# Kernel optimization log

Measured on AMD Instinct MI355X. Metric: run time of the kernel, lower is better.

## Reference

```python
import jax, jax.numpy as jnp
import numpy as np

N_HEADS = 16
N_KV_HEADS = 4
HEAD_DIM = 128  # d_model // n_heads = 2048 // 16
ROPE_THETA = 10000.0


def _rope_cos_sin(T, D, dtype):
    inv_freq = 1.0 / (ROPE_THETA ** (jnp.arange(0, D, 2, dtype=jnp.float32) / D))
    t = jnp.arange(T, dtype=jnp.float32)
    freqs = jnp.outer(t, inv_freq)               # [T, D/2]
    emb = jnp.concatenate([freqs, freqs], axis=-1)  # [T, D]
    return jnp.cos(emb).astype(dtype), jnp.sin(emb).astype(dtype)


def _rotate_half(x):
    x1, x2 = jnp.split(x, 2, axis=-1)
    return jnp.concatenate([-x2, x1], axis=-1)


def setup_inputs() -> dict:
    key = jax.random.key(0)
    k1, k2, k3, k4, k5 = jax.random.split(key, 5)
    B, T, C = 2, 2048, 2048
    H, KV, D = N_HEADS, N_KV_HEADS, HEAD_DIM
    s = 0.02
    return {
        "x": jax.random.normal(k1, (B, T, C), dtype=jnp.float32),
        "Wq": jax.random.normal(k2, (C, H * D), dtype=jnp.float32) * s,
        "Wk": jax.random.normal(k3, (C, KV * D), dtype=jnp.float32) * s,
        "Wv": jax.random.normal(k4, (C, KV * D), dtype=jnp.float32) * s,
        "Wo": jax.random.normal(k5, (H * D, C), dtype=jnp.float32) * s,
    }


def reference(x, Wq, Wk, Wv, Wo):
    B, T, C = x.shape
    H, KV, D = N_HEADS, N_KV_HEADS, HEAD_DIM
    G = H // KV
    scale = D ** -0.5

    q = (x @ Wq).reshape(B, T, H, D).transpose(0, 2, 1, 3)    # [B,H,T,D]
    k = (x @ Wk).reshape(B, T, KV, D).transpose(0, 2, 1, 3)   # [B,KV,T,D]
    v = (x @ Wv).reshape(B, T, KV, D).transpose(0, 2, 1, 3)   # [B,KV,T,D]

    cos, sin = _rope_cos_sin(T, D, x.dtype)  # [T,D] each, broadcasts over B,H
    q = q * cos + _rotate_half(q) * sin
    k = k * cos + _rotate_half(k) * sin

    # repeat_interleave kv heads to match query heads
    k = jnp.repeat(k, G, axis=1)  # [B,H,T,D]
    v = jnp.repeat(v, G, axis=1)  # [B,H,T,D]

    scores = jnp.einsum('bhqd,bhkd->bhqk', q, k) * scale  # [B,H,T,T]
    causal = jnp.tril(jnp.ones((T, T), dtype=bool))
    scores = jnp.where(causal, scores, jnp.finfo(scores.dtype).min)
    attn = jax.nn.softmax(scores, axis=-1)

    out = jnp.einsum('bhqk,bhkd->bhqd', attn, v)           # [B,H,T,D]
    out = out.transpose(0, 2, 1, 3).reshape(B, T, H * D)    # [B,T,C]
    return out @ Wo
```

## Files before the change

kernel.cpp:

```cpp
#include <hip/hip_runtime.h>
#include <cstdint>
#include <cstddef>

typedef __attribute__((ext_vector_type(4))) float f32x4;
typedef __attribute__((ext_vector_type(8))) short s16x8;
typedef __attribute__((ext_vector_type(4))) short s16x4;

#define B_  2
#define T_  2048
#define C_  2048
#define H_  16
#define KV_ 4
#define D_  128
#define M_  4096

static __device__ __forceinline__ float bf2f(ushort u){
  union { float f; uint32_t u; } x; x.u = ((uint32_t)u) << 16; return x.f;
}
static __device__ __forceinline__ ushort f2bf(float f){
  union { float f; uint32_t u; } x; x.f = f;
  uint32_t r = x.u + 0x7FFF + ((x.u >> 16) & 1);
  return (ushort)(r >> 16);
}

static __device__ __forceinline__ void gl_lds16(const ushort* g, ushort* s){
  __builtin_amdgcn_global_load_lds((const __attribute__((address_space(1))) void*)g,
                                   (__attribute__((address_space(3))) void*)s, 16, 0, 0);
}

__global__ void cvt_f32_bf16(const float* __restrict__ in, ushort* __restrict__ out, int n4){
  int idx = blockIdx.x * blockDim.x + threadIdx.x;
  int stride = gridDim.x * blockDim.x;
  for (int i = idx; i < n4; i += stride){
    float4 v = ((const float4*)in)[i];
    s16x4 o;
    o[0] = (short)f2bf(v.x); o[1] = (short)f2bf(v.y);
    o[2] = (short)f2bf(v.z); o[3] = (short)f2bf(v.w);
    ((s16x4*)out)[i] = o;
  }
}

__global__ void transpose_all(const float* __restrict__ Wq, const float* __restrict__ Wk,
                              const float* __restrict__ Wv, const float* __restrict__ Wo,
                              ushort* __restrict__ Wcat, ushort* __restrict__ Wot){
  __shared__ float tile[32][33];
  int bx = blockIdx.x;
  const float* W; ushort* Wt; int N; int n0;
  if (bx < 64)      { W = Wq; Wt = Wcat;                          N = 2048; n0 = bx * 32; }
  else if (bx < 80) { W = Wk; Wt = Wcat + (size_t)2048 * 2048;    N = 512;  n0 = (bx - 64) * 32; }
  else if (bx < 96) { W = Wv; Wt = Wcat + (size_t)2560 * 2048;    N = 512;  n0 = (bx - 80) * 32; }
  else              { W = Wo; Wt = Wot;                           N = 2048; n0 = (bx - 96) * 32; }
  int k0 = blockIdx.y * 32;
  int tx = threadIdx.x, ty = threadIdx.y;
  #pragma unroll
  for (int r = 0; r < 4; r++)
    tile[ty + 8*r][tx] = W[(size_t)(k0 + ty + 8*r) * N + n0 + tx];
  __syncthreads();
  #pragma unroll
  for (int r = 0; r < 4; r++)
    Wt[(size_t)(n0 + ty + 8*r) * 2048 + k0 + tx] = f2bf(tile[tx][ty + 8*r]);
}

template<int MODE>
__global__ __launch_bounds__(512)
void gemm_deep(const ushort* __restrict__ A, const ushort* __restrict__ Bt,
               void* __restrict__ C0, void* __restrict__ C1, void* __restrict__ C2,
               int N, int Kd, int nbx){
  __shared__ __align__(16) ushort Abuf[4][8192];
  __shared__ __align__(16) ushort Bbuf[4][8192];
  int tid = threadIdx.x, w = tid >> 6, l = tid & 63;
  int l15 = l & 15, l4 = l >> 4;

  int cpx = gridDim.x >> 3;
  int logical = (blockIdx.x & 7) * cpx + (blockIdx.x >> 3);
  int bx = logical % nbx, by = logical / nbx;
  int rblk = by * 128, cblk = bx * 128;
  int wm = w & 1, wn = w >> 1;

  int sr = tid >> 3;
  int sc = ((tid & 7) * 8) ^ ((sr & 7) << 3);
  const ushort* gA = A  + (size_t)(rblk + sr) * Kd + sc;
  const ushort* gB = Bt + (size_t)(cblk + sr) * Kd + sc;
  size_t rowK = (size_t)64 * Kd;
  int wb = w * 512;

  auto stage = [&](int t){
    int bsel = t & 3; int koff = t * 64;
    gl_lds16(gA + koff,        &Abuf[bsel][wb]);
    gl_lds16(gA + rowK + koff, &Abuf[bsel][4096 + wb]);
    gl_lds16(gB + koff,        &Bbuf[bsel][wb]);
    gl_lds16(gB + rowK + koff, &Bbuf[bsel][4096 + wb]);
  };

  int arow = wm * 64 + l15;
  int brow = wn * 32 + l15;
  int kx0 = (l4 * 8) ^ ((l15 & 7) << 3);
  int kx1 = (32 + l4 * 8) ^ ((l15 & 7) << 3);

  f32x4 acc[4][2] = {};

  auto phase = [&](int t, int dostage, int vm){
    const ushort* Ab = Abuf[t & 3];
    const ushort* Bb = Bbuf[t & 3];
    s16x8 a[4][2], b[2][2];
    #pragma unroll
    for (int m = 0; m < 4; m++){
      a[m][0] = *(const s16x8*)(Ab + (arow + m*16) * 64 + kx0);
      a[m][1] = *(const s16x8*)(Ab + (arow + m*16) * 64 + kx1);
    }
    #pragma unroll
    for (int n = 0; n < 2; n++){
      b[n][0] = *(const s16x8*)(Bb + (brow + n*16) * 64 + kx0);
      b[n][1] = *(const s16x8*)(Bb + (brow + n*16) * 64 + kx1);
    }
    if (dostage) stage(t + 3);
    if (vm == 8)      { asm volatile("s_waitcnt vmcnt(8)" ::: "memory"); }
    else if (vm == 4) { asm volatile("s_waitcnt vmcnt(4)" ::: "memory"); }
    else if (vm == 0) { asm volatile("s_waitcnt vmcnt(0)" ::: "memory"); }
    asm volatile("s_waitcnt lgkmcnt(0)" ::: "memory");
    __builtin_amdgcn_sched_barrier(0);
    __builtin_amdgcn_s_barrier();
    __builtin_amdgcn_s_setprio(1);
    #pragma unroll
    for (int m = 0; m < 4; m++)
      #pragma unroll
      for (int n = 0; n < 2; n++){
        acc[m][n] = __builtin_amdgcn_mfma_f32_16x16x32_bf16(a[m][0], b[n][0], acc[m][n], 0, 0, 0);
        acc[m][n] = __builtin_amdgcn_mfma_f32_16x16x32_bf16(a[m][1], b[n][1], acc[m][n], 0, 0, 0);
      }
    __builtin_amdgcn_s_setprio(0);
  };

  stage(0); stage(1); stage(2);
  asm volatile("s_waitcnt vmcnt(8)" ::: "memory");
  __builtin_amdgcn_s_barrier();

  int nt = Kd >> 6;
  #pragma unroll 1
  for (int t = 0; t < nt - 3; ++t) phase(t, 1, 8);
  phase(nt - 3, 0, 4);
  phase(nt - 2, 0, 0);
  phase(nt - 1, 0, -1);

  #pragma unroll
  for (int m = 0; m < 4; m++){
    #pragma unroll
    for (int n = 0; n < 2; n++){
      #pragma unroll
      for (int j = 0; j < 4; j++){
        int row = rblk + wm*64 + m*16 + l4*4 + j;
        int col = cblk + wn*32 + n*16 + l15;
        float v = acc[m][n][j];
        if (MODE == 0){
          ((float*)C0)[(size_t)row * N + col] = v;
        } else {
          int t = row & (T_ - 1), bb = row >> 11;
          ushort bv = f2bf(v);
          if (col < 2048){
            int hh = col >> 7, d = col & 127;
            ((ushort*)C0)[(((size_t)(bb * H_ + hh)) * T_ + t) * D_ + d] = bv;
          } else if (col < 2560){
            int c2 = col - 2048;
            int hh = c2 >> 7, d = c2 & 127;
            ((ushort*)C1)[(((size_t)(bb * KV_ + hh)) * T_ + t) * D_ + d] = bv;
          } else {
            int c2 = col - 2560;
            int hh = c2 >> 7, d = c2 & 127;
            ((ushort*)C2)[(((size_t)(bb * KV_ + hh)) * D_ + d) * T_ + t] = bv;
          }
        }
      }
    }
  }
}

__global__ __launch_bounds__(256)
void rope_all(ushort* __restrict__ Qb, ushort* __restrict__ Kb, float sq){
  int y = blockIdx.y;
  ushort* X; int bh; float scale;
  if (y < B_ * H_){ X = Qb; bh = y;           scale = sq;  }
  else            { X = Kb; bh = y - B_ * H_; scale = 1.f; }
  int tr = threadIdx.x >> 4;
  int j  = threadIdx.x & 15;
  int t  = blockIdx.x * 16 + tr;
  ushort* row = X + ((size_t)bh * T_ + t) * D_;
  s16x4 lo = *(const s16x4*)(row + j*4);
  s16x4 hi = *(const s16x4*)(row + 64 + j*4);
  s16x4 olo, ohi;
  #pragma unroll
  for (int i = 0; i < 4; i++){
    int d = j*4 + i;
    float invf = exp2f(-(float)d * 0.2076205059304602f);
    float s, c;
    __sincosf((float)t * invf, &s, &c);
    float q1 = bf2f((ushort)lo[i]);
    float q2 = bf2f((ushort)hi[i]);
    olo[i] = (short)f2bf((q1 * c - q2 * s) * scale);
    ohi[i] = (short)f2bf((q2 * c + q1 * s) * scale);
  }
  *(s16x4*)(row + j*4) = olo;
  *(s16x4*)(row + 64 + j*4) = ohi;
}

__global__ __launch_bounds__(512, 4)
void attn_kernel4(const ushort* __restrict__ Q, const ushort* __restrict__ Kc,
                  const ushort* __restrict__ Vt, ushort* __restrict__ O){
  __shared__ __align__(16) ushort Ks[64 * 128];
  __shared__ __align__(16) ushort Vs[128 * 64];
  __shared__ __align__(16) ushort Ps[8 * 16 * 64];
  int bid = blockIdx.x;
  int i  = bid >> 3;
  int qt = (i < 32) ? (63 - i) : (i - 32);
  int sub = bid & 7;
  int b = sub >> 2, kvh = sub & 3;
  int tid = threadIdx.x, w = tid >> 6, l = tid & 63;
  int l15 = l & 15, l4 = l >> 4;
  int sw3 = (l15 & 7) << 3;
  int q0 = qt * 32;
  int hq = kvh * 4 + (w >> 1);
  int qrow0 = q0 + (w & 1) * 16;
  int qrow = qrow0 + l15;

  s16x8 qf[4];
  const ushort* qbase = Q + (((size_t)(b * H_ + hq)) * T_ + qrow) * D_;
  #pragma unroll
  for (int kk = 0; kk < 4; kk++)
    qf[kk] = *(const s16x8*)(qbase + kk * 32 + l4 * 8);

  f32x4 oacc[8] = {};
  float mrun = -1e30f;
  float rsum = 0.f;
  const float THR = 11.5415603f;
  ushort* Pw = Ps + w * (16 * 64) + l15 * 64;

  const ushort* kbase = Kc + ((size_t)(b * KV_ + kvh)) * T_ * D_;
  const ushort* vbase = Vt + ((size_t)(b * KV_ + kvh)) * D_ * T_;
  int jmax = (q0 + 31) >> 6;

  int kr0 = tid >> 4, kcb = tid & 15;
  int vd0 = tid >> 3, vtb = tid & 7;
  int ksoff = kr0 * 128 + ((kcb * 8) ^ ((kr0 & 7) << 3));
  int vsoff = vd0 * 64  + ((vtb * 8) ^ ((vd0 & 7) << 3));
  const ushort* kg = kbase + (size_t)kr0 * D_ + kcb * 8;
  const ushort* vg = vbase + (size_t)vd0 * T_ + vtb * 8;

  s16x8 kreg0, kreg1, vreg0, vreg1;
  kreg0 = *(const s16x8*)(kg);
  kreg1 = *(const s16x8*)(kg + (size_t)32 * D_);
  vreg0 = *(const s16x8*)(vg);
  vreg1 = *(const s16x8*)(vg + (size_t)64 * T_);

  for (int jt = 0; jt <= jmax; jt++){
    __syncthreads();
    *(s16x8*)(Ks + ksoff)            = kreg0;
    *(s16x8*)(Ks + ksoff + 32 * 128) = kreg1;
    *(s16x8*)(Vs + vsoff)            = vreg0;
    *(s16x8*)(Vs + vsoff + 64 * 64)  = vreg1;
    __syncthreads();
    if (jt < jmax){
      int k1 = (jt + 1) * 64;
      kreg0 = *(const s16x8*)(kg + (size_t)k1 * D_);
      kreg1 = *(const s16x8*)(kg + (size_t)(k1 + 32) * D_);
      vreg0 = *(const s16x8*)(vg + k1);
      vreg1 = *(const s16x8*)(vg + (size_t)64 * T_ + k1);
    }
    int k0 = jt * 64;

    f32x4 sacc[4] = {};
    __builtin_amdgcn_s_setprio(1);
    #pragma unroll
    for (int kk = 0; kk < 4; kk++){
      #pragma unroll
      for (int n = 0; n < 4; n++){
        s16x8 kf = *(const s16x8*)(Ks + (16*n + l15) * 128 + ((kk*32 + l4*8) ^ sw3));
        sacc[n] = __builtin_amdgcn_mfma_f32_16x16x32_bf16(kf, qf[kk], sacc[n], 0, 0, 0);
      }
    }
    __builtin_amdgcn_s_setprio(0);
    if (jt == jmax){
      #pragma unroll
      for (int n = 0; n < 4; n++)
        #pragma unroll
        for (int j = 0; j < 4; j++){
          int kcol = k0 + 16*n + 4*l4 + j;
          if (kcol > qrow) sacc[n][j] = -1e30f;
        }
    }
    float mloc = -1e30f;
    #pragma unroll
    for (int n = 0; n < 4; n++)
      #pragma unroll
      for (int j = 0; j < 4; j++)
        mloc = fmaxf(mloc, sacc[n][j]);
    if (__any((int)(mloc > mrun + THR))){
      float m2 = fmaxf(mloc, __shfl_xor(mloc, 16));
      m2 = fmaxf(m2, __shfl_xor(m2, 32));
      float mnew = fmaxf(mrun, m2);
      float alpha = exp2f(mrun - mnew);
      mrun = mnew;
      rsum *= alpha;
      #pragma unroll
      for (int n8 = 0; n8 < 8; n8++)
        #pragma unroll
        for (int j = 0; j < 4; j++)
          oacc[n8][j] *= alpha;
    }
    #pragma unroll
    for (int n = 0; n < 4; n++){
      float p0 = exp2f(sacc[n][0] - mrun);
      float p1 = exp2f(sacc[n][1] - mrun);
      float p2 = exp2f(sacc[n][2] - mrun);
      float p3 = exp2f(sacc[n][3] - mrun);
      rsum += (p0 + p1) + (p2 + p3);
      uint32_t lo, hi;
      asm volatile("v_cvt_pk_bf16_f32 %0, %1, %2" : "=v"(lo) : "v"(p0), "v"(p1));
      asm volatile("v_cvt_pk_bf16_f32 %0, %1, %2" : "=v"(hi) : "v"(p2), "v"(p3));
      uint2 pk; pk.x = lo; pk.y = hi;
      *(uint2*)(Pw + ((16*n + 4*l4) ^ sw3)) = pk;
    }
    __builtin_amdgcn_s_setprio(1);
    #pragma unroll
    for (int kk = 0; kk < 2; kk++){
      s16x8 pf = *(const s16x8*)(Pw + ((kk*32 + l4*8) ^ sw3));
      #pragma unroll
      for (int n8 = 0; n8 < 8; n8++){
        s16x8 vf = *(const s16x8*)(Vs + (16*n8 + l15) * 64 + ((kk*32 + l4*8) ^ sw3));
        oacc[n8] = __builtin_amdgcn_mfma_f32_16x16x32_bf16(vf, pf, oacc[n8], 0, 0, 0);
      }
    }
    __builtin_amdgcn_s_setprio(0);
  }

  rsum += __shfl_xor(rsum, 16);
  rsum += __shfl_xor(rsum, 32);
  float inv = 1.f / rsum;
  ushort* obase = O + ((size_t)(b * T_ + qrow)) * C_ + hq * D_ + 4*l4;
  #pragma unroll
  for (int n8 = 0; n8 < 8; n8++){
    s16x4 ov;
    #pragma unroll
    for (int j = 0; j < 4; j++)
      ov[j] = (short)f2bf(oacc[n8][j] * inv);
    *(s16x4*)(obase + 16*n8) = ov;
  }
}

extern "C" void kernel_launch(void* const* d_in, const int* in_sizes, int n_in,
                              void* d_out, int out_size, void* d_ws, size_t ws_size,
                              hipStream_t stream){
  const float* x  = (const float*)d_in[0];
  const float* Wq = (const float*)d_in[1];
  const float* Wk = (const float*)d_in[2];
  const float* Wv = (const float*)d_in[3];
  const float* Wo = (const float*)d_in[4];
  float* out = (float*)d_out;

  char* ws = (char*)d_ws;
  size_t off = 0;
  auto alloc = [&](size_t bytes)->void*{
    void* p = ws + off; off += (bytes + 255) & ~(size_t)255; return p;
  };
  ushort* xb   = (ushort*)alloc((size_t)M_ * C_ * 2);
  ushort* Wcat = (ushort*)alloc((size_t)3072 * 2048 * 2);
  ushort* Wot  = (ushort*)alloc((size_t)2048 * 2048 * 2);
  ushort* Qb   = (ushort*)alloc((size_t)B_ * H_ * T_ * D_ * 2);
  ushort* Kb   = (ushort*)alloc((size_t)B_ * KV_ * T_ * D_ * 2);
  ushort* Vtb  = (ushort*)alloc((size_t)B_ * KV_ * T_ * D_ * 2);
  ushort* Ob   = (ushort*)alloc((size_t)M_ * C_ * 2);

  cvt_f32_bf16<<<2048, 256, 0, stream>>>(x, xb, M_ * C_ / 4);
  transpose_all<<<dim3(160, 64), dim3(32, 8), 0, stream>>>(Wq, Wk, Wv, Wo, Wcat, Wot);

  gemm_deep<1><<<768, 512, 0, stream>>>(xb, Wcat, Qb, Kb, Vtb, 3072, 2048, 24);

  rope_all<<<dim3(T_/16, B_ * (H_ + KV_)), 256, 0, stream>>>(
      Qb, Kb, 0.08838834764831845f * 1.4426950408889634f);

  attn_kernel4<<<512, 512, 0, stream>>>(Qb, Kb, Vtb, Ob);

  gemm_deep<0><<<512, 512, 0, stream>>>(Ob, Wot, out, nullptr, nullptr, 2048, 2048, 16);
}
```

Before: 207.5 us.

## Fuse RoPE into QKV GEMM epilogue via permuted weight columns

Permutes the Q and K weight columns during the transpose so each RoPE rotation pair (d, d+64) sits in adjacent output columns. The QKV GEMM epilogue then applies the rotation and the softmax scale with a lane shuffle and sincos before storing. This removes the separate rope kernel and its extra read/write pass over Q and K. The cost is extra transcendental and shuffle work in the GEMM epilogue.

```diff
diff --git a/kernel.cpp b/kernel.cpp
--- a/kernel.cpp
+++ b/kernel.cpp
@@ -45,11 +45,11 @@
                               ushort* __restrict__ Wcat, ushort* __restrict__ Wot){
   __shared__ float tile[32][33];
   int bx = blockIdx.x;
-  const float* W; ushort* Wt; int N; int n0;
-  if (bx < 64)      { W = Wq; Wt = Wcat;                          N = 2048; n0 = bx * 32; }
-  else if (bx < 80) { W = Wk; Wt = Wcat + (size_t)2048 * 2048;    N = 512;  n0 = (bx - 64) * 32; }
-  else if (bx < 96) { W = Wv; Wt = Wcat + (size_t)2560 * 2048;    N = 512;  n0 = (bx - 80) * 32; }
-  else              { W = Wo; Wt = Wot;                           N = 2048; n0 = (bx - 96) * 32; }
+  const float* W; ushort* Wt; int N; int n0; bool perm;
+  if (bx < 64)      { W = Wq; Wt = Wcat;                          N = 2048; n0 = bx * 32;        perm = true;  }
+  else if (bx < 80) { W = Wk; Wt = Wcat + (size_t)2048 * 2048;    N = 512;  n0 = (bx - 64) * 32; perm = true;  }
+  else if (bx < 96) { W = Wv; Wt = Wcat + (size_t)2560 * 2048;    N = 512;  n0 = (bx - 80) * 32; perm = false; }
+  else              { W = Wo; Wt = Wot;                           N = 2048; n0 = (bx - 96) * 32; perm = false; }
   int k0 = blockIdx.y * 32;
   int tx = threadIdx.x, ty = threadIdx.y;
   #pragma unroll
@@ -57,15 +57,18 @@
     tile[ty + 8*r][tx] = W[(size_t)(k0 + ty + 8*r) * N + n0 + tx];
   __syncthreads();
   #pragma unroll
-  for (int r = 0; r < 4; r++)
-    Wt[(size_t)(n0 + ty + 8*r) * 2048 + k0 + tx] = f2bf(tile[tx][ty + 8*r]);
+  for (int r = 0; r < 4; r++){
+    int nn = n0 + ty + 8*r;
+    int dst = perm ? ((nn & ~127) | (((nn & 63) << 1) | ((nn >> 6) & 1))) : nn;
+    Wt[(size_t)dst * 2048 + k0 + tx] = f2bf(tile[tx][ty + 8*r]);
+  }
 }
 
 template<int MODE>
 __global__ __launch_bounds__(512)
 void gemm_deep(const ushort* __restrict__ A, const ushort* __restrict__ Bt,
                void* __restrict__ C0, void* __restrict__ C1, void* __restrict__ C2,
-               int N, int Kd, int nbx){
+               int N, int Kd, int nbx, float sq){
   __shared__ __align__(16) ushort Abuf[4][8192];
   __shared__ __align__(16) ushort Bbuf[4][8192];
   int tid = threadIdx.x, w = tid >> 6, l = tid & 63;
@@ -155,51 +158,33 @@
           ((float*)C0)[(size_t)row * N + col] = v;
         } else {
           int t = row & (T_ - 1), bb = row >> 11;
-          ushort bv = f2bf(v);
-          if (col < 2048){
-            int hh = col >> 7, d = col & 127;
-            ((ushort*)C0)[(((size_t)(bb * H_ + hh)) * T_ + t) * D_ + d] = bv;
-          } else if (col < 2560){
-            int c2 = col - 2048;
-            int hh = c2 >> 7, d = c2 & 127;
-            ((ushort*)C1)[(((size_t)(bb * KV_ + hh)) * T_ + t) * D_ + d] = bv;
+          if (cblk < 2560){
+            int c  = wn*32 + n*16 + l15;
+            int ii = c >> 1;
+            int p  = c & 1;
+            float partner = __shfl_xor(v, 1);
+            float s, co;
+            __sincosf((float)t * exp2f(-(float)ii * 0.2076205059304602f), &s, &co);
+            float o = p ? (v * co + partner * s) : (v * co - partner * s);
+            o *= (cblk < 2048) ? sq : 1.0f;
+            int d = ii + (p << 6);
+            ushort bv = f2bf(o);
+            if (cblk < 2048){
+              int hh = col >> 7;
+              ((ushort*)C0)[(((size_t)(bb * H_ + hh)) * T_ + t) * D_ + d] = bv;
+            } else {
+              int hh = (col - 2048) >> 7;
+              ((ushort*)C1)[(((size_t)(bb * KV_ + hh)) * T_ + t) * D_ + d] = bv;
+            }
           } else {
             int c2 = col - 2560;
             int hh = c2 >> 7, d = c2 & 127;
-            ((ushort*)C2)[(((size_t)(bb * KV_ + hh)) * D_ + d) * T_ + t] = bv;
+            ((ushort*)C2)[(((size_t)(bb * KV_ + hh)) * D_ + d) * T_ + t] = f2bf(v);
           }
         }
       }
     }
   }
-}
-
-__global__ __launch_bounds__(256)
-void rope_all(ushort* __restrict__ Qb, ushort* __restrict__ Kb, float sq){
-  int y = blockIdx.y;
-  ushort* X; int bh; float scale;
-  if (y < B_ * H_){ X = Qb; bh = y;           scale = sq;  }
-  else            { X = Kb; bh = y - B_ * H_; scale = 1.f; }
-  int tr = threadIdx.x >> 4;
-  int j  = threadIdx.x & 15;
-  int t  = blockIdx.x * 16 + tr;
-  ushort* row = X + ((size_t)bh * T_ + t) * D_;
-  s16x4 lo = *(const s16x4*)(row + j*4);
-  s16x4 hi = *(const s16x4*)(row + 64 + j*4);
-  s16x4 olo, ohi;
-  #pragma unroll
-  for (int i = 0; i < 4; i++){
-    int d = j*4 + i;
-    float invf = exp2f(-(float)d * 0.2076205059304602f);
-    float s, c;
-    __sincosf((float)t * invf, &s, &c);
-    float q1 = bf2f((ushort)lo[i]);
-    float q2 = bf2f((ushort)hi[i]);
-    olo[i] = (short)f2bf((q1 * c - q2 * s) * scale);
-    ohi[i] = (short)f2bf((q2 * c + q1 * s) * scale);
-  }
-  *(s16x4*)(row + j*4) = olo;
-  *(s16x4*)(row + 64 + j*4) = ohi;
 }
 
 __global__ __launch_bounds__(512, 4)
@@ -371,12 +356,10 @@
   cvt_f32_bf16<<<2048, 256, 0, stream>>>(x, xb, M_ * C_ / 4);
   transpose_all<<<dim3(160, 64), dim3(32, 8), 0, stream>>>(Wq, Wk, Wv, Wo, Wcat, Wot);
 
-  gemm_deep<1><<<768, 512, 0, stream>>>(xb, Wcat, Qb, Kb, Vtb, 3072, 2048, 24);
-
-  rope_all<<<dim3(T_/16, B_ * (H_ + KV_)), 256, 0, stream>>>(
-      Qb, Kb, 0.08838834764831845f * 1.4426950408889634f);
+  gemm_deep<1><<<768, 512, 0, stream>>>(xb, Wcat, Qb, Kb, Vtb, 3072, 2048, 24,
+                                        0.08838834764831845f * 1.4426950408889634f);
 
   attn_kernel4<<<512, 512, 0, stream>>>(Qb, Kb, Vtb, Ob);
 
-  gemm_deep<0><<<512, 512, 0, stream>>>(Ob, Wot, out, nullptr, nullptr, 2048, 2048, 16);
-}
+  gemm_deep<0><<<512, 512, 0, stream>>>(Ob, Wot, out, nullptr, nullptr, 2048, 2048, 16, 0.f);
+}
```

Measured after the change: 197.6 us. 4.8% less time.
